# Performance work log

Measured on AMD Instinct MI355X. Metric: run time of the kernel, lower is better.

## Reference

```python
import jax, jax.numpy as jnp
import numpy as np

H, W, PART = 16, 16, 4
EPS = 1e-5


def _window_rows(h, part):
    # Static, boundary-clamped window row indices, as in position_aware_max.
    pr = h // part
    half = pr // 2
    idx = []
    for i in range(h):
        u, l = i - half, i + half
        if u < 0:
            u, l = 0, pr
        if l > h:
            u, l = h - pr, h
        idx.append(np.arange(u, l))
    return np.stack(idx)  # [h, pr] (uniform length since pr is even)


def _pam(s6, row_idx, dim):
    # s6: [p, g, hr, wr, hc, wc]; row index r = hr*W + wr, col index s = hc*W + wc.
    if dim == 0:
        # per column block i (hc == i): max over rows hr in window, all wr; keep wc
        sc = jnp.moveaxis(s6, 4, 0)  # [hc, p, g, hr, wr, wc]
        f = lambda sci, idx: jnp.take(sci, idx, axis=2).max(axis=(2, 3))
    else:
        # per row block i (hr == i): max over cols hc in window, all wc; keep wr
        sc = jnp.moveaxis(s6, 2, 0)  # [hr, p, g, wr, hc, wc]
        f = lambda sci, idx: jnp.take(sci, idx, axis=3).max(axis=(3, 4))
    out = jax.vmap(f)(sc, jnp.asarray(row_idx))  # [h, p, g, w]
    p, g = s6.shape[0], s6.shape[1]
    return jnp.transpose(out, (1, 2, 0, 3)).reshape(p, g, -1)  # [p, g, hw]


def _bn(x, gamma, beta, axes):
    # BatchNorm in training mode: biased batch statistics (torch default).
    m = x.mean(axis=axes, keepdims=True)
    v = x.var(axis=axes, keepdims=True)
    return gamma * (x - m) * jax.lax.rsqrt(v + EPS) + beta


def setup_inputs() -> dict:
    key = jax.random.key(0)
    k0, k1, k2 = jax.random.split(key, 3)
    p, g, c = 48, 48, 64
    hw = H * W
    return {
        "prob_fea": jax.random.normal(k0, (p, c, H, W), jnp.float32),
        "gal_fea": jax.random.normal(k1, (g, c, H, W), jnp.float32),
        "bn_gamma": jnp.ones((1,), jnp.float32),
        "bn_beta": jnp.zeros((1,), jnp.float32),
        "fc_w": jnp.full((1, hw), 1.0 / hw, jnp.float32),  # reset_parameters fill
        "fc_b": jax.random.normal(k2, (1,), jnp.float32) * 0.01,
        "lbn_gamma": jnp.ones((1,), jnp.float32),
        "lbn_beta": jnp.zeros((1,), jnp.float32),
    }


def reference(prob_fea, gal_fea, bn_gamma, bn_beta, fc_w, fc_b, lbn_gamma, lbn_beta):
    p, c = prob_fea.shape[0], prob_fea.shape[1]
    g = gal_fea.shape[0]
    hw = H * W
    pf = prob_fea.reshape(p, c, hw)
    gf = gal_fea.reshape(g, c, hw)
    score = jnp.einsum('pcs,gcr->pgrs', pf, gf)  # [p, g, hw, hw]
    s6 = score.reshape(p, g, H, W, H, W)
    row_idx = _window_rows(H, PART)
    s1 = _pam(s6, row_idx, 0)  # [p, g, hw]
    s2 = _pam(s6, row_idx, 1)  # [p, g, hw]
    sc = jnp.concatenate([s1, s2], axis=-1).reshape(-1, 1, hw)  # [2*p*g, 1, hw]
    sc = _bn(sc, bn_gamma, bn_beta, (0, 2)).reshape(-1, hw)
    sc = sc @ fc_w.T + fc_b  # [2*p*g, 1]
    sc = sc.reshape(-1, 2).sum(axis=1, keepdims=True)  # [p*g, 1]
    sc = _bn(sc, lbn_gamma, lbn_beta, (0,))
    return jax.nn.sigmoid(sc).reshape(p, g)
```

## Files before the change

kernel.cpp:

```cpp
#include <hip/hip_runtime.h>

typedef __attribute__((ext_vector_type(8))) short short8;
typedef __attribute__((ext_vector_type(4))) float float4v;

__constant__ int LOW[24] = {0,0,0,1,2,3,4,5,6,7,8,9,10,11,12,12,
                            99,99,99,99,99,99,99,99};
__constant__ int HIW[24] = {3,3,3,4,5,6,7,8,9,10,11,12,13,14,15,15,
                            -1,-1,-1,-1,-1,-1,-1,-1};
__constant__ int CTLO[4] = {0, 2, 6, 10};

__device__ __forceinline__ unsigned short f2bf(float f) {
    unsigned int x = __builtin_bit_cast(unsigned int, f);
    x += 0x7FFF + ((x >> 16) & 1);
    return (unsigned short)(x >> 16);
}

struct __align__(16) U16x8 { unsigned short u[8]; };

template <int CTRL>
__device__ __forceinline__ float dppmaxf(float x) {
    int y = __builtin_amdgcn_update_dpp(0, __builtin_bit_cast(int, x),
                                        CTRL, 0xF, 0xF, true);
    return fmaxf(x, __builtin_bit_cast(float, y));
}
template <int CTRL>
__device__ __forceinline__ float dppaddf(float x) {
    int y = __builtin_amdgcn_update_dpp(0, __builtin_bit_cast(int, x),
                                        CTRL, 0xF, 0xF, true);
    return x + __builtin_bit_cast(float, y);
}
__device__ __forceinline__ float rowmax16(float x) {
    x = dppmaxf<0xB1>(x);
    x = dppmaxf<0x4E>(x);
    x = dppmaxf<0x141>(x);
    x = dppmaxf<0x140>(x);
    return x;
}
__device__ __forceinline__ float rowsum16(float x) {
    x = dppaddf<0xB1>(x);
    x = dppaddf<0x4E>(x);
    x = dppaddf<0x141>(x);
    x = dppaddf<0x140>(x);
    return x;
}

__global__ __launch_bounds__(256) void pretranspose_kernel(
    const float* __restrict__ prob,
    const float* __restrict__ gal,
    unsigned short* __restrict__ outT,
    float* __restrict__ accums)
{
    const int gidx = blockIdx.x * 256 + threadIdx.x;
    if (gidx < 6912) accums[gidx] = 0.0f;

    const int img = blockIdx.x;
    const float* src = (img < 48) ? (prob + img * 16384)
                                  : (gal + (img - 48) * 16384);
    unsigned short* dst = outT + img * 16384;
    const int tid = threadIdx.x;
    const int c0 = (tid & 7) * 8;
    const int s0 = (tid >> 3) * 8;
    unsigned short v[8][8];
#pragma unroll
    for (int i = 0; i < 8; ++i) {
        const float* p = src + (c0 + i) * 256 + s0;
        const float4v f0 = *(const float4v*)(p);
        const float4v f1 = *(const float4v*)(p + 4);
        v[i][0] = f2bf(f0.x); v[i][1] = f2bf(f0.y);
        v[i][2] = f2bf(f0.z); v[i][3] = f2bf(f0.w);
        v[i][4] = f2bf(f1.x); v[i][5] = f2bf(f1.y);
        v[i][6] = f2bf(f1.z); v[i][7] = f2bf(f1.w);
    }
#pragma unroll
    for (int j = 0; j < 8; ++j) {
        U16x8 o;
#pragma unroll
        for (int i = 0; i < 8; ++i) o.u[i] = v[i][j];
        const int srow = s0 + j;
        const int off = srow * 64 + (((c0 >> 3) ^ (srow & 7)) << 3);
        *(U16x8*)(dst + off) = o;
    }
}

__global__ __launch_bounds__(256, 3) void score_pam_kernel(
    const unsigned short* __restrict__ preT,
    const float* __restrict__ fcw,
    float* __restrict__ outDot,
    float* __restrict__ outSum,
    float* __restrict__ outSq)
{
    __shared__ float s1part[4][8][4][16];

    const int tid = threadIdx.x;
    const int pair = blockIdx.x;
    const int ip = pair / 48;
    const int ig = pair % 48;
    const unsigned short* pimg = preT + ip * 16384;
    const unsigned short* gimg = preT + (48 + ig) * 16384;

    const int lane = tid & 63;
    const int w = tid >> 6;
    const int laneM = lane & 15;
    const int q = lane >> 4;
    const int z = laneM & 7;

    const int rtb = 4 * w;
    int lo2[4], hi2[4];
#pragma unroll
    for (int j = 0; j < 4; ++j) { lo2[j] = LOW[rtb + j]; hi2[j] = HIW[rtb + j]; }
    const int ctbase = CTLO[w];

    short8 a0[4], a1[4];
#pragma unroll
    for (int j = 0; j < 4; ++j) {
        const int srow = (rtb + j) * 16 + laneM;
        a0[j] = *(const short8*)(gimg + srow * 64 + ((q ^ z) << 3));
        a1[j] = *(const short8*)(gimg + srow * 64 + (((q + 4) ^ z) << 3));
    }
    short8 B0[8], B1[8];
#pragma unroll
    for (int i = 0; i < 8; ++i) {
        const int ctr = ctbase + i;
        const int ctc = (ctr > 15) ? 15 : ctr;
        const int sl = ctc * 16 + laneM;
        B0[i] = *(const short8*)(pimg + sl * 64 + ((q ^ z) << 3));
        B1[i] = *(const short8*)(pimg + sl * 64 + (((q + 4) ^ z) << 3));
    }

    float4v run[4];
#pragma unroll
    for (int j = 0; j < 4; ++j)
        run[j] = (float4v){ -3.0e38f, -3.0e38f, -3.0e38f, -3.0e38f };
    float s1p[8];
#pragma unroll
    for (int i = 0; i < 8; ++i) s1p[i] = -3.0e38f;

#pragma unroll
    for (int i = 0; i < 8; ++i) {
        const int ctr = ctbase + i;
        const int wl = LOW[ctr], wh = HIW[ctr];
#pragma unroll
        for (int j = 0; j < 4; ++j) {
            const int rt = rtb + j;
            const bool c2 = (ctr >= lo2[j]) && (ctr <= hi2[j]);
            const bool c1 = (rt >= wl) && (rt <= wh);
            if (c1 || c2) {
                float4v acc = { 0.f, 0.f, 0.f, 0.f };
                acc = __builtin_amdgcn_mfma_f32_16x16x32_bf16(a0[j], B0[i], acc, 0, 0, 0);
                acc = __builtin_amdgcn_mfma_f32_16x16x32_bf16(a1[j], B1[i], acc, 0, 0, 0);
                if (c2) {
                    run[j].x = fmaxf(run[j].x, acc.x);
                    run[j].y = fmaxf(run[j].y, acc.y);
                    run[j].z = fmaxf(run[j].z, acc.z);
                    run[j].w = fmaxf(run[j].w, acc.w);
                }
                if (c1) {
                    const float t = fmaxf(fmaxf(acc.x, acc.y), fmaxf(acc.z, acc.w));
                    s1p[i] = fmaxf(s1p[i], t);
                }
            }
        }
    }

    {
        float dot = 0.f, sum = 0.f, sq = 0.f;
#pragma unroll
        for (int j = 0; j < 4; ++j) {
            const float rx = rowmax16(run[j].x);
            const float ry = rowmax16(run[j].y);
            const float rz = rowmax16(run[j].z);
            const float rw = rowmax16(run[j].w);
            const float4v fw = *(const float4v*)(fcw + (rtb + j) * 16 + q * 4);
            dot += rx * fw.x + ry * fw.y + rz * fw.z + rw * fw.w;
            sum += rx + ry + rz + rw;
            sq  += rx * rx + ry * ry + rz * rz + rw * rw;
        }
        if (laneM == 0) {
            atomicAdd(&outDot[pair], dot);
            atomicAdd(&outSum[pair], sum);
            atomicAdd(&outSq[pair], sq);
        }
    }

#pragma unroll
    for (int i = 0; i < 8; ++i) s1part[w][i][q][laneM] = s1p[i];
    __syncthreads();

    {
        const int hc = tid >> 4;
        const int col = tid & 15;
        float v = -3.0e38f;
#pragma unroll
        for (int wv = 0; wv < 4; ++wv) {
            const int ii = hc - CTLO[wv];
            if (ii >= 0 && ii < 8) {
#pragma unroll
                for (int q2 = 0; q2 < 4; ++q2)
                    v = fmaxf(v, s1part[wv][ii][q2][col]);
            }
        }
        float d1 = rowsum16(v * fcw[tid]);
        float s1v = rowsum16(v);
        float q1 = rowsum16(v * v);
        if (laneM == 0) {
            atomicAdd(&outDot[pair], d1);
            atomicAdd(&outSum[pair], s1v);
            atomicAdd(&outSq[pair], q1);
        }
    }
}

__global__ __launch_bounds__(256) void finalize_kernel(
    const float* __restrict__ dDot,
    const float* __restrict__ dSum,
    const float* __restrict__ dSq,
    const float* __restrict__ bng,
    const float* __restrict__ bnb,
    const float* __restrict__ fcw,
    const float* __restrict__ fcb,
    const float* __restrict__ lg,
    const float* __restrict__ lb,
    float* __restrict__ outp)
{
    __shared__ float red[12];
    const int tid = threadIdx.x;
    const int lane = tid & 63;
    const int w = tid >> 6;

    float S = 0.f, Q = 0.f;
    float dv[9];
#pragma unroll
    for (int k = 0; k < 9; ++k) {
        const int i = tid + 256 * k;
        dv[k] = dDot[i];
        S += dSum[i];
        Q += dSq[i];
    }
    float Wj = fcw[tid];
#pragma unroll
    for (int d = 32; d >= 1; d >>= 1) {
        S += __shfl_down(S, d, 64);
        Q += __shfl_down(Q, d, 64);
        Wj += __shfl_down(Wj, d, 64);
    }
    if (lane == 0) { red[w] = S; red[4 + w] = Q; red[8 + w] = Wj; }
    __syncthreads();
    S = red[0] + red[1] + red[2] + red[3];
    Q = red[4] + red[5] + red[6] + red[7];
    const float W = red[8] + red[9] + red[10] + red[11];
    __syncthreads();

    const float N1 = 1179648.0f;
    const float m1 = S / N1;
    const float v1 = Q / N1 - m1 * m1;
    const float inv1 = rsqrtf(v1 + 1e-5f);
    const float g1 = bng[0], b1 = bnb[0], fb = fcb[0];
    const float g2 = lg[0], b2 = lb[0];
    const float cA = g1 * inv1;
    const float cB = 2.f * (b1 * W + fb) - cA * 2.f * m1 * W;

    float Sy = 0.f, Qy = 0.f;
    float yv[9];
#pragma unroll
    for (int k = 0; k < 9; ++k) {
        const float y = cA * dv[k] + cB;
        yv[k] = y;
        Sy += y;
        Qy += y * y;
    }
#pragma unroll
    for (int d = 32; d >= 1; d >>= 1) {
        Sy += __shfl_down(Sy, d, 64);
        Qy += __shfl_down(Qy, d, 64);
    }
    if (lane == 0) { red[w] = Sy; red[4 + w] = Qy; }
    __syncthreads();
    Sy = red[0] + red[1] + red[2] + red[3];
    Qy = red[4] + red[5] + red[6] + red[7];

    const float m2 = Sy / 2304.0f;
    const float v2 = Qy / 2304.0f - m2 * m2;
    const float inv2 = rsqrtf(v2 + 1e-5f);
#pragma unroll
    for (int k = 0; k < 9; ++k) {
        const int i = tid + 256 * k;
        const float z = g2 * (yv[k] - m2) * inv2 + b2;
        outp[i] = 1.0f / (1.0f + __expf(-z));
    }
}

extern "C" void kernel_launch(void* const* d_in, const int* in_sizes, int n_in,
                              void* d_out, int out_size, void* d_ws, size_t ws_size,
                              hipStream_t stream) {
    const float* prob = (const float*)d_in[0];
    const float* gal  = (const float*)d_in[1];
    const float* bng  = (const float*)d_in[2];
    const float* bnb  = (const float*)d_in[3];
    const float* fcw  = (const float*)d_in[4];
    const float* fcb  = (const float*)d_in[5];
    const float* lg   = (const float*)d_in[6];
    const float* lb   = (const float*)d_in[7];

    unsigned short* preT = (unsigned short*)d_ws;
    float* ws = (float*)((char*)d_ws + 96 * 16384 * sizeof(unsigned short));
    float* dDot = ws;
    float* dSum = ws + 2304;
    float* dSq  = ws + 4608;

    hipLaunchKernelGGL(pretranspose_kernel, dim3(96), dim3(256), 0, stream,
                       prob, gal, preT, dDot);
    hipLaunchKernelGGL(score_pam_kernel, dim3(48 * 48), dim3(256), 0, stream,
                       preT, fcw, dDot, dSum, dSq);
    hipLaunchKernelGGL(finalize_kernel, dim3(1), dim3(256), 0, stream,
                       dDot, dSum, dSq, bng, bnb, fcw, fcb, lg, lb,
                       (float*)d_out);
}
```

Baseline: 108.0 us.

## Process three gallery images per block and replace atomics with shared-memory reduction

Each block now handles one probe image and three gallery images, so the probe fragments (B0/B1) and fc weights are loaded once and reused across three pairs. The grid shrinks from 2304 to 768 blocks. The per-pair global atomicAdds are replaced by an in-block reduction through shared memory followed by plain stores, which also removes the need to zero the accumulators in the pretranspose kernel. In exchange there are extra __syncthreads per pair and fewer blocks to spread across the GPU.

```diff
diff --git a/kernel.cpp b/kernel.cpp
--- a/kernel.cpp
+++ b/kernel.cpp
@@ -47,12 +47,8 @@
 __global__ __launch_bounds__(256) void pretranspose_kernel(
     const float* __restrict__ prob,
     const float* __restrict__ gal,
-    unsigned short* __restrict__ outT,
-    float* __restrict__ accums)
+    unsigned short* __restrict__ outT)
 {
-    const int gidx = blockIdx.x * 256 + threadIdx.x;
-    if (gidx < 6912) accums[gidx] = 0.0f;
-
     const int img = blockIdx.x;
     const float* src = (img < 48) ? (prob + img * 16384)
                                   : (gal + (img - 48) * 16384);
@@ -90,13 +86,13 @@
     float* __restrict__ outSq)
 {
     __shared__ float s1part[4][8][4][16];
+    __shared__ float redA[4][4][4];
+    __shared__ float redB[4][4];
 
     const int tid = threadIdx.x;
-    const int pair = blockIdx.x;
-    const int ip = pair / 48;
-    const int ig = pair % 48;
+    const int ip = blockIdx.x >> 4;
+    const int grp = blockIdx.x & 15;
     const unsigned short* pimg = preT + ip * 16384;
-    const unsigned short* gimg = preT + (48 + ig) * 16384;
 
     const int lane = tid & 63;
     const int w = tid >> 6;
@@ -110,13 +106,6 @@
     for (int j = 0; j < 4; ++j) { lo2[j] = LOW[rtb + j]; hi2[j] = HIW[rtb + j]; }
     const int ctbase = CTLO[w];
 
-    short8 a0[4], a1[4];
-#pragma unroll
-    for (int j = 0; j < 4; ++j) {
-        const int srow = (rtb + j) * 16 + laneM;
-        a0[j] = *(const short8*)(gimg + srow * 64 + ((q ^ z) << 3));
-        a1[j] = *(const short8*)(gimg + srow * 64 + (((q + 4) ^ z) << 3));
-    }
     short8 B0[8], B1[8];
 #pragma unroll
     for (int i = 0; i < 8; ++i) {
@@ -126,86 +115,116 @@
         B0[i] = *(const short8*)(pimg + sl * 64 + ((q ^ z) << 3));
         B1[i] = *(const short8*)(pimg + sl * 64 + (((q + 4) ^ z) << 3));
     }
-
-    float4v run[4];
+    float4v fw[4];
 #pragma unroll
     for (int j = 0; j < 4; ++j)
-        run[j] = (float4v){ -3.0e38f, -3.0e38f, -3.0e38f, -3.0e38f };
-    float s1p[8];
-#pragma unroll
-    for (int i = 0; i < 8; ++i) s1p[i] = -3.0e38f;
-
-#pragma unroll
-    for (int i = 0; i < 8; ++i) {
-        const int ctr = ctbase + i;
-        const int wl = LOW[ctr], wh = HIW[ctr];
+        fw[j] = *(const float4v*)(fcw + (rtb + j) * 16 + q * 4);
+    const float fcw_t = fcw[tid];
+
+    for (int k = 0; k < 3; ++k) {
+        const int ig = 3 * grp + k;
+        const int pair = ip * 48 + ig;
+        const unsigned short* gimg = preT + (48 + ig) * 16384;
+
+        short8 a0[4], a1[4];
 #pragma unroll
         for (int j = 0; j < 4; ++j) {
-            const int rt = rtb + j;
-            const bool c2 = (ctr >= lo2[j]) && (ctr <= hi2[j]);
-            const bool c1 = (rt >= wl) && (rt <= wh);
-            if (c1 || c2) {
-                float4v acc = { 0.f, 0.f, 0.f, 0.f };
-                acc = __builtin_amdgcn_mfma_f32_16x16x32_bf16(a0[j], B0[i], acc, 0, 0, 0);
-                acc = __builtin_amdgcn_mfma_f32_16x16x32_bf16(a1[j], B1[i], acc, 0, 0, 0);
-                if (c2) {
-                    run[j].x = fmaxf(run[j].x, acc.x);
-                    run[j].y = fmaxf(run[j].y, acc.y);
-                    run[j].z = fmaxf(run[j].z, acc.z);
-                    run[j].w = fmaxf(run[j].w, acc.w);
-                }
-                if (c1) {
-                    const float t = fmaxf(fmaxf(acc.x, acc.y), fmaxf(acc.z, acc.w));
-                    s1p[i] = fmaxf(s1p[i], t);
+            const int srow = (rtb + j) * 16 + laneM;
+            a0[j] = *(const short8*)(gimg + srow * 64 + ((q ^ z) << 3));
+            a1[j] = *(const short8*)(gimg + srow * 64 + (((q + 4) ^ z) << 3));
+        }
+
+        float4v run[4];
+#pragma unroll
+        for (int j = 0; j < 4; ++j)
+            run[j] = (float4v){ -3.0e38f, -3.0e38f, -3.0e38f, -3.0e38f };
+        float s1p[8];
+#pragma unroll
+        for (int i = 0; i < 8; ++i) s1p[i] = -3.0e38f;
+
+#pragma unroll
+        for (int i = 0; i < 8; ++i) {
+            const int ctr = ctbase + i;
+            const int wl = LOW[ctr], wh = HIW[ctr];
+#pragma unroll
+            for (int j = 0; j < 4; ++j) {
+                const int rt = rtb + j;
+                const bool c2 = (ctr >= lo2[j]) && (ctr <= hi2[j]);
+                const bool c1 = (rt >= wl) && (rt <= wh);
+                if (c1 || c2) {
+                    float4v acc = { 0.f, 0.f, 0.f, 0.f };
+                    acc = __builtin_amdgcn_mfma_f32_16x16x32_bf16(a0[j], B0[i], acc, 0, 0, 0);
+                    acc = __builtin_amdgcn_mfma_f32_16x16x32_bf16(a1[j], B1[i], acc, 0, 0, 0);
+                    if (c2) {
+                        run[j].x = fmaxf(run[j].x, acc.x);
+                        run[j].y = fmaxf(run[j].y, acc.y);
+                        run[j].z = fmaxf(run[j].z, acc.z);
+                        run[j].w = fmaxf(run[j].w, acc.w);
+                    }
+                    if (c1) {
+                        const float t = fmaxf(fmaxf(acc.x, acc.y), fmaxf(acc.z, acc.w));
+                        s1p[i] = fmaxf(s1p[i], t);
+                    }
                 }
             }
         }
-    }
-
-    {
+
         float dot = 0.f, sum = 0.f, sq = 0.f;
+        const float msk = (laneM == 0) ? 1.0f : 0.0f;
 #pragma unroll
         for (int j = 0; j < 4; ++j) {
             const float rx = rowmax16(run[j].x);
             const float ry = rowmax16(run[j].y);
             const float rz = rowmax16(run[j].z);
             const float rw = rowmax16(run[j].w);
-            const float4v fw = *(const float4v*)(fcw + (rtb + j) * 16 + q * 4);
-            dot += rx * fw.x + ry * fw.y + rz * fw.z + rw * fw.w;
-            sum += rx + ry + rz + rw;
-            sq  += rx * rx + ry * ry + rz * rz + rw * rw;
-        }
-        if (laneM == 0) {
-            atomicAdd(&outDot[pair], dot);
-            atomicAdd(&outSum[pair], sum);
-            atomicAdd(&outSq[pair], sq);
-        }
-    }
-
-#pragma unroll
-    for (int i = 0; i < 8; ++i) s1part[w][i][q][laneM] = s1p[i];
-    __syncthreads();
-
-    {
-        const int hc = tid >> 4;
-        const int col = tid & 15;
-        float v = -3.0e38f;
-#pragma unroll
-        for (int wv = 0; wv < 4; ++wv) {
-            const int ii = hc - CTLO[wv];
-            if (ii >= 0 && ii < 8) {
-#pragma unroll
-                for (int q2 = 0; q2 < 4; ++q2)
-                    v = fmaxf(v, s1part[wv][ii][q2][col]);
+            float t;
+            t = msk * rx; dot += t * fw[j].x; sum += t; sq += t * rx;
+            t = msk * ry; dot += t * fw[j].y; sum += t; sq += t * ry;
+            t = msk * rz; dot += t * fw[j].z; sum += t; sq += t * rz;
+            t = msk * rw; dot += t * fw[j].w; sum += t; sq += t * rw;
+        }
+
+        __syncthreads();
+        if (laneM == 0) { redA[w][q][0] = dot; redA[w][q][1] = sum; redA[w][q][2] = sq; }
+#pragma unroll
+        for (int i = 0; i < 8; ++i) s1part[w][i][q][laneM] = s1p[i];
+        __syncthreads();
+
+        {
+            const int hc = tid >> 4;
+            const int col = tid & 15;
+            float v = -3.0e38f;
+#pragma unroll
+            for (int wv = 0; wv < 4; ++wv) {
+                const int ii = hc - CTLO[wv];
+                if (ii >= 0 && ii < 8) {
+#pragma unroll
+                    for (int q2 = 0; q2 < 4; ++q2)
+                        v = fmaxf(v, s1part[wv][ii][q2][col]);
+                }
             }
-        }
-        float d1 = rowsum16(v * fcw[tid]);
-        float s1v = rowsum16(v);
-        float q1 = rowsum16(v * v);
-        if (laneM == 0) {
-            atomicAdd(&outDot[pair], d1);
-            atomicAdd(&outSum[pair], s1v);
-            atomicAdd(&outSq[pair], q1);
+            float d1 = rowsum16(v * fcw_t);
+            float s1v = rowsum16(v);
+            float q1 = rowsum16(v * v);
+            d1 += __shfl_xor(d1, 16, 64);  s1v += __shfl_xor(s1v, 16, 64);
+            q1 += __shfl_xor(q1, 16, 64);
+            d1 += __shfl_xor(d1, 32, 64);  s1v += __shfl_xor(s1v, 32, 64);
+            q1 += __shfl_xor(q1, 32, 64);
+            if (lane == 0) { redB[w][0] = d1; redB[w][1] = s1v; redB[w][2] = q1; }
+        }
+        __syncthreads();
+
+        if (tid < 3) {
+            float s = 0.f;
+#pragma unroll
+            for (int a = 0; a < 4; ++a) {
+#pragma unroll
+                for (int b = 0; b < 4; ++b) s += redA[a][b][tid];
+                s += redB[a][tid];
+            }
+            if (tid == 0) outDot[pair] = s;
+            else if (tid == 1) outSum[pair] = s;
+            else outSq[pair] = s;
         }
     }
 }
@@ -308,8 +327,8 @@
     float* dSq  = ws + 4608;
 
     hipLaunchKernelGGL(pretranspose_kernel, dim3(96), dim3(256), 0, stream,
-                       prob, gal, preT, dDot);
-    hipLaunchKernelGGL(score_pam_kernel, dim3(48 * 48), dim3(256), 0, stream,
+                       prob, gal, preT);
+    hipLaunchKernelGGL(score_pam_kernel, dim3(768), dim3(256), 0, stream,
                        preT, fcw, dDot, dSum, dSq);
     hipLaunchKernelGGL(finalize_kernel, dim3(1), dim3(256), 0, stream,
                        dDot, dSum, dSq, bng, bnb, fcw, fcb, lg, lb,
```

New measurement: 99.31 us. -8.1%, faster.
